# Kernel tuning notes

Hardware: AMD Instinct MI355X
Metric: run time of the kernel (lower is better)

Reference implementation:

```python
import jax, jax.numpy as jnp
import numpy as np

N_NODES = 468  # MediaPipe face-mesh landmark count


def build_edges(n):
    # static edge structure from create_face_graph: i <-> j for j in i+1..min(i+10, n)
    src, dst = [], []
    for i in range(n):
        for j in range(i + 1, min(i + 10, n)):
            src += [i, j]
            dst += [j, i]
    # PyG GCNConv adds self-loops before normalization
    src = np.asarray(src + list(range(n)), dtype=np.int32)
    dst = np.asarray(dst + list(range(n)), dtype=np.int32)
    deg = np.bincount(dst, minlength=n).astype(np.float32)
    dinv = 1.0 / np.sqrt(deg)
    norm = (dinv[src] * dinv[dst]).astype(np.float32)
    return jnp.asarray(src), jnp.asarray(dst), jnp.asarray(norm)


def gcn_conv(x, W, b, src, dst, norm):
    # x: [B, N, d_in] -> [B, N, d_out]; GCNConv: transform then normalized scatter-add
    h = x @ W                                   # [B, N, d_out]
    msg = h[:, src, :] * norm[None, :, None]    # gather along node dim: [B, E, d_out]
    agg = jnp.zeros_like(h).at[:, dst, :].add(msg)
    return agg + b


def setup_inputs() -> dict:
    key = jax.random.key(0)
    ks = jax.random.split(key, 13)
    s = 0.05
    inp = {
        'landmarks': jax.random.normal(ks[0], (128, N_NODES * 3), dtype=jnp.float32),
        'W_enc': jax.random.normal(ks[1], (3, 64), dtype=jnp.float32) * s,
        'b_enc': jnp.zeros((64,), dtype=jnp.float32),
        'W1': jax.random.normal(ks[2], (64, 128), dtype=jnp.float32) * s,
        'b1': jnp.zeros((128,), dtype=jnp.float32),
        'W2': jax.random.normal(ks[3], (128, 256), dtype=jnp.float32) * s,
        'b2': jnp.zeros((256,), dtype=jnp.float32),
        'W3': jax.random.normal(ks[4], (256, 128), dtype=jnp.float32) * s,
        'b3': jnp.zeros((128,), dtype=jnp.float32),
        'W_fus': jax.random.normal(ks[5], (128, 512), dtype=jnp.float32) * s,
        'b_fus': jnp.zeros((512,), dtype=jnp.float32),
        'W_cls': jax.random.normal(ks[6], (512, 2), dtype=jnp.float32) * s,
        'b_cls': jnp.zeros((2,), dtype=jnp.float32),
    }
    return inp


def reference(landmarks, W_enc, b_enc, W1, b1, W2, b2, W3, b3, W_fus, b_fus, W_cls, b_cls):
    B = landmarks.shape[0]
    n = landmarks.shape[1] // 3
    src, dst, norm = build_edges(n)
    x = landmarks.reshape(B, n, 3) @ W_enc + b_enc            # node encoder [B,N,64]
    x = jax.nn.relu(gcn_conv(x, W1, b1, src, dst, norm))      # [B,N,128]
    x = jax.nn.relu(gcn_conv(x, W2, b2, src, dst, norm))      # [B,N,256]
    x = jax.nn.relu(gcn_conv(x, W3, b3, src, dst, norm))      # [B,N,128]
    graph_features = jnp.mean(x, axis=1)                      # global mean pool [B,128]
    features = jax.nn.relu(graph_features @ W_fus + b_fus)    # fusion (dropout=eval) [B,512]
    output = features @ W_cls + b_cls                         # classifier [B,2]
    return output, features, graph_features
```

## Files before the change

### kernel.cpp

```cpp
#include <hip/hip_runtime.h>
#include <hip/hip_bf16.h>

typedef __bf16 bf16x8 __attribute__((ext_vector_type(8)));
typedef float  f32x4  __attribute__((ext_vector_type(4)));
typedef unsigned short ushort_t;

#define NN 468

#define W1H 0
#define W1L 8192
#define W2H 16384
#define W2L 49152
#define W3H 81920
#define W3L 114688

#define L_Y1   32096
#define L_Y2   27200
#define L_Y3   43296
#define L_LM   76352
#define L_DTAB 77768
#define L_POOL 78240

#define MFMA3(d, ah, al, wh, wl)                                        \
    d = __builtin_amdgcn_mfma_f32_16x16x32_bf16(ah, wh, d, 0, 0, 0);    \
    d = __builtin_amdgcn_mfma_f32_16x16x32_bf16(ah, wl, d, 0, 0, 0);    \
    d = __builtin_amdgcn_mfma_f32_16x16x32_bf16(al, wh, d, 0, 0, 0);

__device__ __forceinline__ void pack_split4(const float* y,
                                            ushort_t* hdst, ushort_t* ldst) {
    ushort_t h[4], l[4];
    #pragma unroll
    for (int j = 0; j < 4; ++j) {
        __hip_bfloat16 hb = __float2bfloat16(y[j]);
        float hf = __bfloat162float(hb);
        __hip_bfloat16 lb = __float2bfloat16(y[j] - hf);
        h[j] = *(ushort_t*)&hb; l[j] = *(ushort_t*)&lb;
    }
    uint2 hv = make_uint2((unsigned)h[0] | ((unsigned)h[1] << 16),
                          (unsigned)h[2] | ((unsigned)h[3] << 16));
    uint2 lv = make_uint2((unsigned)l[0] | ((unsigned)l[1] << 16),
                          (unsigned)l[2] | ((unsigned)l[3] << 16));
    *(uint2*)hdst = hv;
    *(uint2*)ldst = lv;
}

__device__ __forceinline__ int frag_off(int r, int k, int K16) {
    return (r >> 4) * K16 + (k >> 5) * 512 + ((k >> 3) & 3) * 128
         + (r & 15) * 8 + (k & 7);
}

__device__ __forceinline__ int ywoff(int r, int k4, int K16) {
    int q = (k4 >> 3) & 3;
    int u = q * 16 + (((r & 15) ^ (q << 1)) & 15);
    return (r >> 4) * K16 + (k4 >> 5) * 512 + u * 8 + (k4 & 7);
}

__global__ __launch_bounds__(512, 4) void fused(
    const float* __restrict__ Lm, const ushort_t* __restrict__ wext,
    const float* __restrict__ We, const float* __restrict__ be,
    const float* __restrict__ b1, const float* __restrict__ b2,
    const float* __restrict__ b3, float* __restrict__ partial)
{
    __shared__ __align__(16) char lds[78752];
    float*    X    = (float*)(lds);
    ushort_t* Y1h  = (ushort_t*)(lds + L_Y1);  ushort_t* Y1l = Y1h + 7168;
    ushort_t* Y2h  = (ushort_t*)(lds + L_Y2);  ushort_t* Y2l = Y2h + 12288;
    ushort_t* Y3h  = (ushort_t*)(lds + L_Y3);  ushort_t* Y3l = Y3h + 8192;
    float*    lmst = (float*)(lds + L_LM);
    float*    dtab = (float*)(lds + L_DTAB);
    float*    pool = (float*)(lds + L_POOL);

    const int tid  = threadIdx.x;
    const int lane = tid & 63;
    const int wave = tid >> 6;
    const int wm = wave & 1, wn = wave >> 1;
    const int l15 = lane & 15, lg = lane >> 4;
    const int lswz = (lane & 48) + (((lane & 15) ^ ((lane >> 4) << 1)) & 15);
    const int rt = blockIdx.x, b = blockIdx.y;
    const int r0 = rt * 64;

    if (tid < 118) {
        int ri = r0 - 27 + tid;
        float dv = 0.f;
        if (ri >= 0 && ri < NN) {
            int lo = ri - 9; if (lo < 0) lo = 0;
            int hi = ri + 9; if (hi > NN - 1) hi = NN - 1;
            dv = 1.0f / sqrtf((float)(hi - lo + 1));
        }
        dtab[tid] = dv;
    }
    if (tid < 354) {
        int g = (r0 - 27) * 3 + tid;
        lmst[tid] = (g >= 0 && g < NN * 3) ? Lm[(size_t)b * (NN * 3) + g] : 0.f;
    }
    if (tid < 128) pool[tid] = 0.f;
    __syncthreads();

    {
        const int c = tid & 63;
        const float w0 = We[c], w1 = We[64 + c], w2 = We[128 + c], bk = be[c];
        for (int l0 = tid >> 6; l0 < 118; l0 += 8) {
            float x = bk + lmst[l0*3]*w0 + lmst[l0*3+1]*w1 + lmst[l0*3+2]*w2;
            X[l0 * 68 + c] = x * dtab[l0];
        }
    }
    __syncthreads();

    {
        const int c4 = (tid & 15) << 2;
        const int base = (tid >> 4) * 4;
        if (base < 100) {
            f32x4 ws = {};
            #pragma unroll
            for (int d = 0; d < 19; ++d)
                ws += *(const f32x4*)(X + (base + d) * 68 + c4);
            #pragma unroll
            for (int rr = 0; rr < 4; ++rr) {
                int row = base + rr;
                if (rr) ws += *(const f32x4*)(X + (row + 18) * 68 + c4)
                            - *(const f32x4*)(X + (row - 1)  * 68 + c4);
                float dv = dtab[row + 9];
                float y4[4] = {ws[0]*dv, ws[1]*dv, ws[2]*dv, ws[3]*dv};
                int off = ywoff(row, c4, 1024);
                pack_split4(y4, Y1h + off, Y1l + off);
            }
        } else if (base < 112) {
            float z4[4] = {0.f, 0.f, 0.f, 0.f};
            #pragma unroll
            for (int rr = 0; rr < 4; ++rr) {
                int row = base + rr;
                if (row < 112) {
                    int off = ywoff(row, c4, 1024);
                    pack_split4(z4, Y1h + off, Y1l + off);
                }
            }
        }
    }
    __syncthreads();

    f32x4 acc1[4][2] = {};
    __builtin_amdgcn_s_setprio(1);
    #pragma unroll
    for (int kt = 0; kt < 2; ++kt) {
        bf16x8 a[4][2];
        #pragma unroll
        for (int mt = 0; mt < 4; ++mt) {
            int t = wm*4 + mt; if (t > 6) t = 6;
            int off = t * 1024 + kt * 512 + lswz * 8;
            a[mt][0] = *(const bf16x8*)(Y1h + off);
            a[mt][1] = *(const bf16x8*)(Y1l + off);
        }
        #pragma unroll
        for (int nt = 0; nt < 2; ++nt) {
            int woff = (nt*4 + wn) * 1024 + kt * 512 + lane * 8;
            bf16x8 wh = *(const bf16x8*)(wext + W1H + woff);
            bf16x8 wl = *(const bf16x8*)(wext + W1L + woff);
            #pragma unroll
            for (int mt = 0; mt < 4; ++mt) {
                MFMA3(acc1[mt][nt], a[mt][0], a[mt][1], wh, wl);
            }
        }
    }
    __builtin_amdgcn_s_setprio(0);

    #pragma unroll
    for (int kc = 0; kc < 2; ++kc) {
        #pragma unroll
        for (int mt = 0; mt < 4; ++mt) {
            int t = wm*4 + mt; if (t > 6) t = 6;
            int gcol = (kc*4 + wn)*16 + l15;
            int cl   = wn*16 + l15;
            float bv = b1[gcol];
            #pragma unroll
            for (int r = 0; r < 4; ++r) {
                int lr1 = t*16 + lg*4 + r;
                if (lr1 < 100)
                    X[lr1*68 + cl] =
                        dtab[lr1 + 9] * fmaxf(acc1[mt][kc][r] + bv, 0.f);
            }
        }
        __syncthreads();

        {
            const int c4   = (tid & 15) << 2;
            const int base = (tid >> 4) * 3;
            f32x4 ws = {};
            if (base < 82) {
                #pragma unroll
                for (int d = 0; d < 19; ++d)
                    ws += *(const f32x4*)(X + (base + d) * 68 + c4);
            }
            #pragma unroll
            for (int rr = 0; rr < 3; ++rr) {
                int row = base + rr;
                if (row < 96) {
                    float y4[4] = {0.f, 0.f, 0.f, 0.f};
                    if (row < 82) {
                        if (rr) ws += *(const f32x4*)(X + (row + 18) * 68 + c4)
                                    - *(const f32x4*)(X + (row - 1)  * 68 + c4);
                        float dv = dtab[row + 18];
                        y4[0] = ws[0]*dv; y4[1] = ws[1]*dv;
                        y4[2] = ws[2]*dv; y4[3] = ws[3]*dv;
                    }
                    int off = ywoff(row, kc*64 + c4, 2048);
                    pack_split4(y4, Y2h + off, Y2l + off);
                }
            }
        }
        __syncthreads();
    }

    f32x4 acc2[3][4] = {};
    __builtin_amdgcn_s_setprio(1);
    #pragma unroll
    for (int kt = 0; kt < 4; ++kt) {
        bf16x8 a[3][2];
        #pragma unroll
        for (int mt = 0; mt < 3; ++mt) {
            int off = (wm*3 + mt) * 2048 + kt * 512 + lswz * 8;
            a[mt][0] = *(const bf16x8*)(Y2h + off);
            a[mt][1] = *(const bf16x8*)(Y2l + off);
        }
        #pragma unroll
        for (int nt = 0; nt < 4; ++nt) {
            int woff = (nt*4 + wn) * 2048 + kt * 512 + lane * 8;
            bf16x8 wh = *(const bf16x8*)(wext + W2H + woff);
            bf16x8 wl = *(const bf16x8*)(wext + W2L + woff);
            #pragma unroll
            for (int mt = 0; mt < 3; ++mt) {
                MFMA3(acc2[mt][nt], a[mt][0], a[mt][1], wh, wl);
            }
        }
    }
    __builtin_amdgcn_s_setprio(0);
    __syncthreads();

    f32x4 acc3[2][2] = {};
    #pragma unroll
    for (int nc = 0; nc < 2; ++nc) {
        if (nc == 1) {
            __builtin_amdgcn_s_setprio(1);
            #pragma unroll
            for (int kt = 0; kt < 4; ++kt) {
                bf16x8 a0[2], a1[2];
                #pragma unroll
                for (int mt = 0; mt < 2; ++mt) {
                    int aoff = (wm*2 + mt) * 2048 + kt * 512 + lswz * 8;
                    a0[mt] = *(const bf16x8*)(Y3h + aoff);
                    a1[mt] = *(const bf16x8*)(Y3l + aoff);
                }
                #pragma unroll
                for (int nt = 0; nt < 2; ++nt) {
                    int woff = (nt*4 + wn) * 4096 + (0*4 + kt) * 512 + lane * 8;
                    bf16x8 wh = *(const bf16x8*)(wext + W3H + woff);
                    bf16x8 wl = *(const bf16x8*)(wext + W3L + woff);
                    #pragma unroll
                    for (int mt = 0; mt < 2; ++mt) {
                        MFMA3(acc3[mt][nt], a0[mt], a1[mt], wh, wl);
                    }
                }
            }
            __builtin_amdgcn_s_setprio(0);
        }
        #pragma unroll
        for (int mt = 0; mt < 3; ++mt)
        #pragma unroll
        for (int q = 0; q < 2; ++q) {
            int gcol = ((nc*2 + q)*4 + wn)*16 + l15;
            int cl   = (q*4 + wn)*16 + l15;
            float bv = b2[gcol];
            #pragma unroll
            for (int r = 0; r < 4; ++r) {
                int lr2 = (wm*3 + mt)*16 + lg*4 + r;
                if (lr2 < 82)
                    X[lr2*132 + cl] =
                        dtab[lr2 + 18] * fmaxf(acc2[mt][nc*2 + q][r] + bv, 0.f);
            }
        }
        __syncthreads();

        {
            const int c4   = (tid & 31) << 2;
            const int base = (tid >> 5) * 4;
            f32x4 ws = {};
            #pragma unroll
            for (int d = 0; d < 19; ++d)
                ws += *(const f32x4*)(X + (base + d) * 132 + c4);
            #pragma unroll
            for (int rr = 0; rr < 4; ++rr) {
                int row = base + rr;
                if (rr) ws += *(const f32x4*)(X + (row + 18) * 132 + c4)
                            - *(const f32x4*)(X + (row - 1)  * 132 + c4);
                float dv = dtab[row + 27];
                float y4[4] = {ws[0]*dv, ws[1]*dv, ws[2]*dv, ws[3]*dv};
                int off = ywoff(row, c4, 2048);
                pack_split4(y4, Y3h + off, Y3l + off);
            }
        }
        __syncthreads();
    }

    __builtin_amdgcn_s_setprio(1);
    #pragma unroll
    for (int kt = 0; kt < 4; ++kt) {
        bf16x8 a0[2], a1[2];
        #pragma unroll
        for (int mt = 0; mt < 2; ++mt) {
            int aoff = (wm*2 + mt) * 2048 + kt * 512 + lswz * 8;
            a0[mt] = *(const bf16x8*)(Y3h + aoff);
            a1[mt] = *(const bf16x8*)(Y3l + aoff);
        }
        #pragma unroll
        for (int nt = 0; nt < 2; ++nt) {
            int woff = (nt*4 + wn) * 4096 + (1*4 + kt) * 512 + lane * 8;
            bf16x8 wh = *(const bf16x8*)(wext + W3H + woff);
            bf16x8 wl = *(const bf16x8*)(wext + W3L + woff);
            #pragma unroll
            for (int mt = 0; mt < 2; ++mt) {
                MFMA3(acc3[mt][nt], a0[mt], a1[mt], wh, wl);
            }
        }
    }
    __builtin_amdgcn_s_setprio(0);

    #pragma unroll
    for (int nt = 0; nt < 2; ++nt) {
        int g_t = nt*4 + wn;
        float bv = b3[g_t*16 + l15];
        float cs = 0.f;
        #pragma unroll
        for (int mt = 0; mt < 2; ++mt)
        #pragma unroll
        for (int r = 0; r < 4; ++r) {
            int gr = r0 + (wm*2 + mt)*16 + lg*4 + r;
            if (gr < NN) cs += fmaxf(acc3[mt][nt][r] + bv, 0.f);
        }
        cs += __shfl_xor(cs, 16);
        cs += __shfl_xor(cs, 32);
        if (lane < 16) atomicAdd(&pool[g_t*16 + lane], cs);
    }
    __syncthreads();
    if (tid < 128) partial[((size_t)b * 8 + rt) * 128 + tid] = pool[tid];
}

__global__ __launch_bounds__(256) void wconv(
    const float* __restrict__ W1, const float* __restrict__ W2,
    const float* __restrict__ W3, ushort_t* __restrict__ wext)
{
    int i = blockIdx.x * 256 + threadIdx.x;
    float w; int off_h, off_l, idx;
    if (i < 8192) {
        int k = i >> 7, n = i & 127;
        w = W1[i]; idx = frag_off(n, k, 1024);  off_h = W1H; off_l = W1L;
    } else if (i < 40960) {
        int j = i - 8192;
        int k = j >> 8, n = j & 255;
        w = W2[j]; idx = frag_off(n, k, 2048);  off_h = W2H; off_l = W2L;
    } else if (i < 73728) {
        int j = i - 40960;
        int k = j >> 7, n = j & 127;
        w = W3[j]; idx = frag_off(n, k, 4096);  off_h = W3H; off_l = W3L;
    } else return;
    __hip_bfloat16 hb = __float2bfloat16(w);
    float hf = __bfloat162float(hb);
    __hip_bfloat16 lb = __float2bfloat16(w - hf);
    wext[off_h + idx] = *(ushort_t*)&hb;
    wext[off_l + idx] = *(ushort_t*)&lb;
}

__global__ __launch_bounds__(512) void head_kernel(
    const float* __restrict__ partial, const float* __restrict__ Wf,
    const float* __restrict__ bf, const float* __restrict__ Wc,
    const float* __restrict__ bc, float* __restrict__ dout)
{
    __shared__ float gfs[128];
    __shared__ float feats[512];
    int b = blockIdx.x, t = threadIdx.x;
    if (t < 128) {
        const float* p = partial + (size_t)b * (8 * 128);
        float s = 0.f;
        #pragma unroll
        for (int tt = 0; tt < 8; ++tt) s += p[tt * 128 + t];
        s *= (1.0f / 468.0f);
        gfs[t] = s;
        dout[65792 + b * 128 + t] = s;
    }
    __syncthreads();
    float a = bf[t];
    for (int k = 0; k < 128; ++k) a += gfs[k] * Wf[k * 512 + t];
    a = fmaxf(a, 0.f);
    dout[256 + b * 512 + t] = a;
    feats[t] = a;
    __syncthreads();
    if (t < 64) {
        float s0 = 0.f, s1 = 0.f;
        for (int c = t; c < 512; c += 64) {
            float f = feats[c];
            s0 += f * Wc[c * 2 + 0];
            s1 += f * Wc[c * 2 + 1];
        }
        #pragma unroll
        for (int off = 32; off; off >>= 1) {
            s0 += __shfl_down(s0, off);
            s1 += __shfl_down(s1, off);
        }
        if (t == 0) {
            dout[b * 2 + 0] = s0 + bc[0];
            dout[b * 2 + 1] = s1 + bc[1];
        }
    }
}

extern "C" void kernel_launch(void* const* d_in, const int* in_sizes, int n_in,
                              void* d_out, int out_size, void* d_ws, size_t ws_size,
                              hipStream_t stream)
{
    const float* landmarks = (const float*)d_in[0];
    const float* W_enc     = (const float*)d_in[1];
    const float* b_enc     = (const float*)d_in[2];
    const float* W1        = (const float*)d_in[3];
    const float* b1        = (const float*)d_in[4];
    const float* W2        = (const float*)d_in[5];
    const float* b2        = (const float*)d_in[6];
    const float* W3        = (const float*)d_in[7];
    const float* b3        = (const float*)d_in[8];
    const float* W_fus     = (const float*)d_in[9];
    const float* b_fus     = (const float*)d_in[10];
    const float* W_cls     = (const float*)d_in[11];
    const float* b_cls     = (const float*)d_in[12];
    float* out = (float*)d_out;

    char* ws = (char*)d_ws;
    ushort_t* wext = (ushort_t*)(ws + 0);
    float* partial = (float*)(ws + 294912);

    wconv<<<288, 256, 0, stream>>>(W1, W2, W3, wext);
    fused<<<dim3(8, 128), 512, 0, stream>>>(
        landmarks, wext, W_enc, b_enc, b1, b2, b3, partial);
    head_kernel<<<128, 512, 0, stream>>>(partial, W_fus, b_fus, W_cls, b_cls, out);
}
```

Baseline: 66.79 us.

## Process two batch samples per block with interleaved software-pipelined phases

Each block now handles two batch elements, with double LDS buffers, and interleaves the phases of the two samples so one sample's GEMM runs alongside the other's band/epilogue work between barriers. The aim is to hide the LDS/ALU phases behind MFMA work and cut the number of barrier-serialized stalls per sample. The cost is doubled LDS (about 157KB, so one block per CU), more live accumulators, and half the grid size, which may reduce occupancy and latency hiding.

```diff
diff --git a/kernel.cpp b/kernel.cpp
--- a/kernel.cpp
+++ b/kernel.cpp
@@ -14,12 +14,14 @@
 #define W3H 81920
 #define W3L 114688
 
-#define L_Y1   32096
-#define L_Y2   27200
-#define L_Y3   43296
-#define L_LM   76352
-#define L_DTAB 77768
-#define L_POOL 78240
+#define UO_Y1 32096
+#define UO_Y2 27200
+#define UO_Y3 43296
+#define UO_LM 76352
+#define U_STRIDE 77768
+#define L_DTAB  (2*U_STRIDE)
+#define L_POOLA (L_DTAB + 472)
+#define L_POOLB (L_POOLA + 512)
 
 #define MFMA3(d, ah, al, wh, wl)                                        \
     d = __builtin_amdgcn_mfma_f32_16x16x32_bf16(ah, wh, d, 0, 0, 0);    \
@@ -55,31 +57,11 @@
     return (r >> 4) * K16 + (k4 >> 5) * 512 + u * 8 + (k4 & 7);
 }
 
-__global__ __launch_bounds__(512, 4) void fused(
-    const float* __restrict__ Lm, const ushort_t* __restrict__ wext,
-    const float* __restrict__ We, const float* __restrict__ be,
-    const float* __restrict__ b1, const float* __restrict__ b2,
-    const float* __restrict__ b3, float* __restrict__ partial)
-{
-    __shared__ __align__(16) char lds[78752];
-    float*    X    = (float*)(lds);
-    ushort_t* Y1h  = (ushort_t*)(lds + L_Y1);  ushort_t* Y1l = Y1h + 7168;
-    ushort_t* Y2h  = (ushort_t*)(lds + L_Y2);  ushort_t* Y2l = Y2h + 12288;
-    ushort_t* Y3h  = (ushort_t*)(lds + L_Y3);  ushort_t* Y3l = Y3h + 8192;
-    float*    lmst = (float*)(lds + L_LM);
-    float*    dtab = (float*)(lds + L_DTAB);
-    float*    pool = (float*)(lds + L_POOL);
-
-    const int tid  = threadIdx.x;
-    const int lane = tid & 63;
-    const int wave = tid >> 6;
-    const int wm = wave & 1, wn = wave >> 1;
-    const int l15 = lane & 15, lg = lane >> 4;
-    const int lswz = (lane & 48) + (((lane & 15) ^ ((lane >> 4) << 1)) & 15);
-    const int rt = blockIdx.x, b = blockIdx.y;
-    const int r0 = rt * 64;
-
-    if (tid < 118) {
+__device__ __forceinline__ void ph_stage(const float* Lm, float* lmst,
+                                         float* pool, float* dtab, bool do_dtab,
+                                         int b, int r0) {
+    int tid = threadIdx.x;
+    if (do_dtab && tid < 118) {
         int ri = r0 - 27 + tid;
         float dv = 0.f;
         if (ri >= 0 && ri < NN) {
@@ -94,51 +76,59 @@
         lmst[tid] = (g >= 0 && g < NN * 3) ? Lm[(size_t)b * (NN * 3) + g] : 0.f;
     }
     if (tid < 128) pool[tid] = 0.f;
-    __syncthreads();
-
-    {
-        const int c = tid & 63;
-        const float w0 = We[c], w1 = We[64 + c], w2 = We[128 + c], bk = be[c];
-        for (int l0 = tid >> 6; l0 < 118; l0 += 8) {
-            float x = bk + lmst[l0*3]*w0 + lmst[l0*3+1]*w1 + lmst[l0*3+2]*w2;
-            X[l0 * 68 + c] = x * dtab[l0];
-        }
-    }
-    __syncthreads();
-
-    {
-        const int c4 = (tid & 15) << 2;
-        const int base = (tid >> 4) * 4;
-        if (base < 100) {
-            f32x4 ws = {};
-            #pragma unroll
-            for (int d = 0; d < 19; ++d)
-                ws += *(const f32x4*)(X + (base + d) * 68 + c4);
-            #pragma unroll
-            for (int rr = 0; rr < 4; ++rr) {
-                int row = base + rr;
-                if (rr) ws += *(const f32x4*)(X + (row + 18) * 68 + c4)
-                            - *(const f32x4*)(X + (row - 1)  * 68 + c4);
-                float dv = dtab[row + 9];
-                float y4[4] = {ws[0]*dv, ws[1]*dv, ws[2]*dv, ws[3]*dv};
+}
+
+__device__ __forceinline__ void ph_enc(float* X, const float* lmst,
+                                       const float* dtab, const float* We,
+                                       const float* be) {
+    int tid = threadIdx.x;
+    const int c = tid & 63;
+    const float w0 = We[c], w1 = We[64 + c], w2 = We[128 + c], bk = be[c];
+    for (int l0 = tid >> 6; l0 < 118; l0 += 8) {
+        float x = bk + lmst[l0*3]*w0 + lmst[l0*3+1]*w1 + lmst[l0*3+2]*w2;
+        X[l0 * 68 + c] = x * dtab[l0];
+    }
+}
+
+__device__ __forceinline__ void ph_band1(const float* X, ushort_t* Y1h,
+                                         ushort_t* Y1l, const float* dtab) {
+    int tid = threadIdx.x;
+    const int c4 = (tid & 15) << 2;
+    const int base = (tid >> 4) * 4;
+    if (base < 100) {
+        f32x4 ws = {};
+        #pragma unroll
+        for (int d = 0; d < 19; ++d)
+            ws += *(const f32x4*)(X + (base + d) * 68 + c4);
+        #pragma unroll
+        for (int rr = 0; rr < 4; ++rr) {
+            int row = base + rr;
+            if (rr) ws += *(const f32x4*)(X + (row + 18) * 68 + c4)
+                        - *(const f32x4*)(X + (row - 1)  * 68 + c4);
+            float dv = dtab[row + 9];
+            float y4[4] = {ws[0]*dv, ws[1]*dv, ws[2]*dv, ws[3]*dv};
+            int off = ywoff(row, c4, 1024);
+            pack_split4(y4, Y1h + off, Y1l + off);
+        }
+    } else if (base < 112) {
+        float z4[4] = {0.f, 0.f, 0.f, 0.f};
+        #pragma unroll
+        for (int rr = 0; rr < 4; ++rr) {
+            int row = base + rr;
+            if (row < 112) {
                 int off = ywoff(row, c4, 1024);
-                pack_split4(y4, Y1h + off, Y1l + off);
+                pack_split4(z4, Y1h + off, Y1l + off);
             }
-        } else if (base < 112) {
-            float z4[4] = {0.f, 0.f, 0.f, 0.f};
-            #pragma unroll
-            for (int rr = 0; rr < 4; ++rr) {
-                int row = base + rr;
-                if (row < 112) {
-                    int off = ywoff(row, c4, 1024);
-                    pack_split4(z4, Y1h + off, Y1l + off);
-                }
-            }
-        }
-    }
-    __syncthreads();
-
-    f32x4 acc1[4][2] = {};
+        }
+    }
+}
+
+__device__ __forceinline__ void ph_gemm1(const ushort_t* Y1h, const ushort_t* Y1l,
+                                         const ushort_t* wext, f32x4 (&acc1)[4][2]) {
+    int tid = threadIdx.x;
+    const int lane = tid & 63, wave = tid >> 6;
+    const int wm = wave & 1, wn = wave >> 1;
+    const int lswz = (lane & 48) + (((lane & 15) ^ ((lane >> 4) << 1)) & 15);
     __builtin_amdgcn_s_setprio(1);
     #pragma unroll
     for (int kt = 0; kt < 2; ++kt) {
@@ -162,55 +152,64 @@
         }
     }
     __builtin_amdgcn_s_setprio(0);
-
-    #pragma unroll
-    for (int kc = 0; kc < 2; ++kc) {
-        #pragma unroll
-        for (int mt = 0; mt < 4; ++mt) {
-            int t = wm*4 + mt; if (t > 6) t = 6;
-            int gcol = (kc*4 + wn)*16 + l15;
-            int cl   = wn*16 + l15;
-            float bv = b1[gcol];
-            #pragma unroll
-            for (int r = 0; r < 4; ++r) {
-                int lr1 = t*16 + lg*4 + r;
-                if (lr1 < 100)
-                    X[lr1*68 + cl] =
-                        dtab[lr1 + 9] * fmaxf(acc1[mt][kc][r] + bv, 0.f);
+}
+
+__device__ __forceinline__ void ph_epi1(float* X, const f32x4 (&acc1)[4][2],
+                                        const float* dtab, const float* b1, int kc) {
+    int tid = threadIdx.x;
+    const int lane = tid & 63, wave = tid >> 6;
+    const int wm = wave & 1, wn = wave >> 1;
+    const int l15 = lane & 15, lg = lane >> 4;
+    #pragma unroll
+    for (int mt = 0; mt < 4; ++mt) {
+        int t = wm*4 + mt; if (t > 6) t = 6;
+        int gcol = (kc*4 + wn)*16 + l15;
+        int cl   = wn*16 + l15;
+        float bv = b1[gcol];
+        #pragma unroll
+        for (int r = 0; r < 4; ++r) {
+            int lr1 = t*16 + lg*4 + r;
+            if (lr1 < 100)
+                X[lr1*68 + cl] = dtab[lr1 + 9] * fmaxf(acc1[mt][kc][r] + bv, 0.f);
+        }
+    }
+}
+
+__device__ __forceinline__ void ph_band2(const float* X, ushort_t* Y2h,
+                                         ushort_t* Y2l, const float* dtab, int kc) {
+    int tid = threadIdx.x;
+    const int c4   = (tid & 15) << 2;
+    const int base = (tid >> 4) * 3;
+    f32x4 ws = {};
+    if (base < 82) {
+        #pragma unroll
+        for (int d = 0; d < 19; ++d)
+            ws += *(const f32x4*)(X + (base + d) * 68 + c4);
+    }
+    #pragma unroll
+    for (int rr = 0; rr < 3; ++rr) {
+        int row = base + rr;
+        if (row < 96) {
+            float y4[4] = {0.f, 0.f, 0.f, 0.f};
+            if (row < 82) {
+                if (rr) ws += *(const f32x4*)(X + (row + 18) * 68 + c4)
+                            - *(const f32x4*)(X + (row - 1)  * 68 + c4);
+                float dv = dtab[row + 18];
+                y4[0] = ws[0]*dv; y4[1] = ws[1]*dv;
+                y4[2] = ws[2]*dv; y4[3] = ws[3]*dv;
             }
-        }
-        __syncthreads();
-
-        {
-            const int c4   = (tid & 15) << 2;
-            const int base = (tid >> 4) * 3;
-            f32x4 ws = {};
-            if (base < 82) {
-                #pragma unroll
-                for (int d = 0; d < 19; ++d)
-                    ws += *(const f32x4*)(X + (base + d) * 68 + c4);
-            }
-            #pragma unroll
-            for (int rr = 0; rr < 3; ++rr) {
-                int row = base + rr;
-                if (row < 96) {
-                    float y4[4] = {0.f, 0.f, 0.f, 0.f};
-                    if (row < 82) {
-                        if (rr) ws += *(const f32x4*)(X + (row + 18) * 68 + c4)
-                                    - *(const f32x4*)(X + (row - 1)  * 68 + c4);
-                        float dv = dtab[row + 18];
-                        y4[0] = ws[0]*dv; y4[1] = ws[1]*dv;
-                        y4[2] = ws[2]*dv; y4[3] = ws[3]*dv;
-                    }
-                    int off = ywoff(row, kc*64 + c4, 2048);
-                    pack_split4(y4, Y2h + off, Y2l + off);
-                }
-            }
-        }
-        __syncthreads();
-    }
-
-    f32x4 acc2[3][4] = {};
+            int off = ywoff(row, kc*64 + c4, 2048);
+            pack_split4(y4, Y2h + off, Y2l + off);
+        }
+    }
+}
+
+__device__ __forceinline__ void ph_gemm2(const ushort_t* Y2h, const ushort_t* Y2l,
+                                         const ushort_t* wext, f32x4 (&acc2)[3][4]) {
+    int tid = threadIdx.x;
+    const int lane = tid & 63, wave = tid >> 6;
+    const int wm = wave & 1, wn = wave >> 1;
+    const int lswz = (lane & 48) + (((lane & 15) ^ ((lane >> 4) << 1)) & 15);
     __builtin_amdgcn_s_setprio(1);
     #pragma unroll
     for (int kt = 0; kt < 4; ++kt) {
@@ -233,73 +232,58 @@
         }
     }
     __builtin_amdgcn_s_setprio(0);
-    __syncthreads();
-
-    f32x4 acc3[2][2] = {};
-    #pragma unroll
-    for (int nc = 0; nc < 2; ++nc) {
-        if (nc == 1) {
-            __builtin_amdgcn_s_setprio(1);
-            #pragma unroll
-            for (int kt = 0; kt < 4; ++kt) {
-                bf16x8 a0[2], a1[2];
-                #pragma unroll
-                for (int mt = 0; mt < 2; ++mt) {
-                    int aoff = (wm*2 + mt) * 2048 + kt * 512 + lswz * 8;
-                    a0[mt] = *(const bf16x8*)(Y3h + aoff);
-                    a1[mt] = *(const bf16x8*)(Y3l + aoff);
-                }
-                #pragma unroll
-                for (int nt = 0; nt < 2; ++nt) {
-                    int woff = (nt*4 + wn) * 4096 + (0*4 + kt) * 512 + lane * 8;
-                    bf16x8 wh = *(const bf16x8*)(wext + W3H + woff);
-                    bf16x8 wl = *(const bf16x8*)(wext + W3L + woff);
-                    #pragma unroll
-                    for (int mt = 0; mt < 2; ++mt) {
-                        MFMA3(acc3[mt][nt], a0[mt], a1[mt], wh, wl);
-                    }
-                }
-            }
-            __builtin_amdgcn_s_setprio(0);
-        }
-        #pragma unroll
-        for (int mt = 0; mt < 3; ++mt)
-        #pragma unroll
-        for (int q = 0; q < 2; ++q) {
-            int gcol = ((nc*2 + q)*4 + wn)*16 + l15;
-            int cl   = (q*4 + wn)*16 + l15;
-            float bv = b2[gcol];
-            #pragma unroll
-            for (int r = 0; r < 4; ++r) {
-                int lr2 = (wm*3 + mt)*16 + lg*4 + r;
-                if (lr2 < 82)
-                    X[lr2*132 + cl] =
-                        dtab[lr2 + 18] * fmaxf(acc2[mt][nc*2 + q][r] + bv, 0.f);
-            }
-        }
-        __syncthreads();
-
-        {
-            const int c4   = (tid & 31) << 2;
-            const int base = (tid >> 5) * 4;
-            f32x4 ws = {};
-            #pragma unroll
-            for (int d = 0; d < 19; ++d)
-                ws += *(const f32x4*)(X + (base + d) * 132 + c4);
-            #pragma unroll
-            for (int rr = 0; rr < 4; ++rr) {
-                int row = base + rr;
-                if (rr) ws += *(const f32x4*)(X + (row + 18) * 132 + c4)
-                            - *(const f32x4*)(X + (row - 1)  * 132 + c4);
-                float dv = dtab[row + 27];
-                float y4[4] = {ws[0]*dv, ws[1]*dv, ws[2]*dv, ws[3]*dv};
-                int off = ywoff(row, c4, 2048);
-                pack_split4(y4, Y3h + off, Y3l + off);
-            }
-        }
-        __syncthreads();
-    }
-
+}
+
+__device__ __forceinline__ void ph_epi2(float* X, const f32x4 (&acc2)[3][4],
+                                        const float* dtab, const float* b2, int nc) {
+    int tid = threadIdx.x;
+    const int lane = tid & 63, wave = tid >> 6;
+    const int wm = wave & 1, wn = wave >> 1;
+    const int l15 = lane & 15, lg = lane >> 4;
+    #pragma unroll
+    for (int mt = 0; mt < 3; ++mt)
+    #pragma unroll
+    for (int q = 0; q < 2; ++q) {
+        int gcol = ((nc*2 + q)*4 + wn)*16 + l15;
+        int cl   = (q*4 + wn)*16 + l15;
+        float bv = b2[gcol];
+        #pragma unroll
+        for (int r = 0; r < 4; ++r) {
+            int lr2 = (wm*3 + mt)*16 + lg*4 + r;
+            if (lr2 < 82)
+                X[lr2*132 + cl] = dtab[lr2 + 18] * fmaxf(acc2[mt][nc*2 + q][r] + bv, 0.f);
+        }
+    }
+}
+
+__device__ __forceinline__ void ph_band3(const float* X, ushort_t* Y3h,
+                                         ushort_t* Y3l, const float* dtab) {
+    int tid = threadIdx.x;
+    const int c4   = (tid & 31) << 2;
+    const int base = (tid >> 5) * 4;
+    f32x4 ws = {};
+    #pragma unroll
+    for (int d = 0; d < 19; ++d)
+        ws += *(const f32x4*)(X + (base + d) * 132 + c4);
+    #pragma unroll
+    for (int rr = 0; rr < 4; ++rr) {
+        int row = base + rr;
+        if (rr) ws += *(const f32x4*)(X + (row + 18) * 132 + c4)
+                    - *(const f32x4*)(X + (row - 1)  * 132 + c4);
+        float dv = dtab[row + 27];
+        float y4[4] = {ws[0]*dv, ws[1]*dv, ws[2]*dv, ws[3]*dv};
+        int off = ywoff(row, c4, 2048);
+        pack_split4(y4, Y3h + off, Y3l + off);
+    }
+}
+
+__device__ __forceinline__ void ph_gemm3(const ushort_t* Y3h, const ushort_t* Y3l,
+                                         const ushort_t* wext, f32x4 (&acc3)[2][2],
+                                         int nc) {
+    int tid = threadIdx.x;
+    const int lane = tid & 63, wave = tid >> 6;
+    const int wm = wave & 1, wn = wave >> 1;
+    const int lswz = (lane & 48) + (((lane & 15) ^ ((lane >> 4) << 1)) & 15);
     __builtin_amdgcn_s_setprio(1);
     #pragma unroll
     for (int kt = 0; kt < 4; ++kt) {
@@ -312,7 +296,7 @@
         }
         #pragma unroll
         for (int nt = 0; nt < 2; ++nt) {
-            int woff = (nt*4 + wn) * 4096 + (1*4 + kt) * 512 + lane * 8;
+            int woff = (nt*4 + wn) * 4096 + (nc*4 + kt) * 512 + lane * 8;
             bf16x8 wh = *(const bf16x8*)(wext + W3H + woff);
             bf16x8 wl = *(const bf16x8*)(wext + W3L + woff);
             #pragma unroll
@@ -322,7 +306,15 @@
         }
     }
     __builtin_amdgcn_s_setprio(0);
-
+}
+
+__device__ __forceinline__ void ph_pool(const f32x4 (&acc3)[2][2], float* pool,
+                                        const float* b3, float* partial,
+                                        int b, int rt, int r0) {
+    int tid = threadIdx.x;
+    const int lane = tid & 63, wave = tid >> 6;
+    const int wm = wave & 1, wn = wave >> 1;
+    const int l15 = lane & 15, lg = lane >> 4;
     #pragma unroll
     for (int nt = 0; nt < 2; ++nt) {
         int g_t = nt*4 + wn;
@@ -341,6 +333,72 @@
     }
     __syncthreads();
     if (tid < 128) partial[((size_t)b * 8 + rt) * 128 + tid] = pool[tid];
+}
+
+__global__ __launch_bounds__(512, 2) void fused2(
+    const float* __restrict__ Lm, const ushort_t* __restrict__ wext,
+    const float* __restrict__ We, const float* __restrict__ be,
+    const float* __restrict__ b1, const float* __restrict__ b2,
+    const float* __restrict__ b3, float* __restrict__ partial)
+{
+    __shared__ __align__(16) char lds[157056];
+    char* uA = lds;
+    char* uB = lds + U_STRIDE;
+    float*    XA   = (float*)(uA);
+    ushort_t* Y1hA = (ushort_t*)(uA + UO_Y1);  ushort_t* Y1lA = Y1hA + 7168;
+    ushort_t* Y2hA = (ushort_t*)(uA + UO_Y2);  ushort_t* Y2lA = Y2hA + 12288;
+    ushort_t* Y3hA = (ushort_t*)(uA + UO_Y3);  ushort_t* Y3lA = Y3hA + 8192;
+    float*    lmA  = (float*)(uA + UO_LM);
+    float*    XB   = (float*)(uB);
+    ushort_t* Y1hB = (ushort_t*)(uB + UO_Y1);  ushort_t* Y1lB = Y1hB + 7168;
+    ushort_t* Y2hB = (ushort_t*)(uB + UO_Y2);  ushort_t* Y2lB = Y2hB + 12288;
+    ushort_t* Y3hB = (ushort_t*)(uB + UO_Y3);  ushort_t* Y3lB = Y3hB + 8192;
+    float*    lmB  = (float*)(uB + UO_LM);
+    float*    dtab = (float*)(lds + L_DTAB);
+    float*    poolA = (float*)(lds + L_POOLA);
+    float*    poolB = (float*)(lds + L_POOLB);
+
+    const int rt = blockIdx.x;
+    const int bA = blockIdx.y * 2, bB = bA + 1;
+    const int r0 = rt * 64;
+
+    f32x4 acc1A[4][2] = {}; f32x4 acc2A[3][4] = {}; f32x4 acc3A[2][2] = {};
+    f32x4 acc1B[4][2] = {}; f32x4 acc2B[3][4] = {}; f32x4 acc3B[2][2] = {};
+
+    #define BAR __syncthreads()
+    ph_stage(Lm, lmA, poolA, dtab, true, bA, r0);                    BAR;
+    ph_enc(XA, lmA, dtab, We, be);                                   BAR;
+    ph_band1(XA, Y1hA, Y1lA, dtab);                                  BAR;
+    ph_gemm1(Y1hA, Y1lA, wext, acc1A);                               BAR;
+    ph_epi1(XA, acc1A, dtab, b1, 0);                                 BAR;
+    ph_band2(XA, Y2hA, Y2lA, dtab, 0);
+    ph_stage(Lm, lmB, poolB, dtab, false, bB, r0);                   BAR;
+    ph_epi1(XA, acc1A, dtab, b1, 1);
+    ph_enc(XB, lmB, dtab, We, be);                                   BAR;
+    ph_band2(XA, Y2hA, Y2lA, dtab, 1);
+    ph_band1(XB, Y1hB, Y1lB, dtab);                                  BAR;
+    ph_gemm2(Y2hA, Y2lA, wext, acc2A);
+    ph_gemm1(Y1hB, Y1lB, wext, acc1B);                               BAR;
+    ph_epi2(XA, acc2A, dtab, b2, 0);
+    ph_epi1(XB, acc1B, dtab, b1, 0);                                 BAR;
+    ph_band3(XA, Y3hA, Y3lA, dtab);
+    ph_band2(XB, Y2hB, Y2lB, dtab, 0);                               BAR;
+    ph_gemm3(Y3hA, Y3lA, wext, acc3A, 0);
+    ph_epi1(XB, acc1B, dtab, b1, 1);                                 BAR;
+    ph_epi2(XA, acc2A, dtab, b2, 1);
+    ph_band2(XB, Y2hB, Y2lB, dtab, 1);                               BAR;
+    ph_band3(XA, Y3hA, Y3lA, dtab);
+    ph_gemm2(Y2hB, Y2lB, wext, acc2B);                               BAR;
+    ph_gemm3(Y3hA, Y3lA, wext, acc3A, 1);
+    ph_epi2(XB, acc2B, dtab, b2, 0);                                 BAR;
+    ph_pool(acc3A, poolA, b3, partial, bA, rt, r0);
+    ph_band3(XB, Y3hB, Y3lB, dtab);                                  BAR;
+    ph_gemm3(Y3hB, Y3lB, wext, acc3B, 0);                            BAR;
+    ph_epi2(XB, acc2B, dtab, b2, 1);                                 BAR;
+    ph_band3(XB, Y3hB, Y3lB, dtab);                                  BAR;
+    ph_gemm3(Y3hB, Y3lB, wext, acc3B, 1);                            BAR;
+    ph_pool(acc3B, poolB, b3, partial, bB, rt, r0);
+    #undef BAR
 }
 
 __global__ __launch_bounds__(256) void wconv(
@@ -435,7 +493,7 @@
     float* partial = (float*)(ws + 294912);
 
     wconv<<<288, 256, 0, stream>>>(W1, W2, W3, wext);
-    fused<<<dim3(8, 128), 512, 0, stream>>>(
+    fused2<<<dim3(8, 64), 512, 0, stream>>>(
         landmarks, wext, W_enc, b_enc, b1, b2, b3, partial);
     head_kernel<<<128, 512, 0, stream>>>(partial, W_fus, b_fus, W_cls, b_cls, out);
 }
```

Result: slower. 148.1 us (+121.8%).

## Double fused kernel block size to 1024 threads, splitting N-tiles across waves

Applied to the files above, without the earlier changes.

Raises the fused GCN kernel from 512 to 1024 threads per block, so 16 waves each own half as many output column tiles in every MFMA stage and half as many rows in the sliding-window aggregation passes. The aim is more parallelism and latency hiding per block, with fewer accumulator registers per thread. The cost is lower possible blocks per CU given the large LDS footprint and the register limit that launch_bounds(1024,4) imposes, and more waves contending at each barrier. Some stages, such as the layer-1 epilogue, now leave half the waves idle.

```diff
diff --git a/kernel.cpp b/kernel.cpp
--- a/kernel.cpp
+++ b/kernel.cpp
@@ -55,7 +55,7 @@
     return (r >> 4) * K16 + (k4 >> 5) * 512 + u * 8 + (k4 & 7);
 }
 
-__global__ __launch_bounds__(512, 4) void fused(
+__global__ __launch_bounds__(1024, 4) void fused(
     const float* __restrict__ Lm, const ushort_t* __restrict__ wext,
     const float* __restrict__ We, const float* __restrict__ be,
     const float* __restrict__ b1, const float* __restrict__ b2,
@@ -99,7 +99,7 @@
     {
         const int c = tid & 63;
         const float w0 = We[c], w1 = We[64 + c], w2 = We[128 + c], bk = be[c];
-        for (int l0 = tid >> 6; l0 < 118; l0 += 8) {
+        for (int l0 = tid >> 6; l0 < 118; l0 += 16) {
             float x = bk + lmst[l0*3]*w0 + lmst[l0*3+1]*w1 + lmst[l0*3+2]*w2;
             X[l0 * 68 + c] = x * dtab[l0];
         }
@@ -108,14 +108,14 @@
 
     {
         const int c4 = (tid & 15) << 2;
-        const int base = (tid >> 4) * 4;
+        const int base = (tid >> 4) * 2;
         if (base < 100) {
             f32x4 ws = {};
             #pragma unroll
             for (int d = 0; d < 19; ++d)
                 ws += *(const f32x4*)(X + (base + d) * 68 + c4);
             #pragma unroll
-            for (int rr = 0; rr < 4; ++rr) {
+            for (int rr = 0; rr < 2; ++rr) {
                 int row = base + rr;
                 if (rr) ws += *(const f32x4*)(X + (row + 18) * 68 + c4)
                             - *(const f32x4*)(X + (row - 1)  * 68 + c4);
@@ -127,7 +127,7 @@
         } else if (base < 112) {
             float z4[4] = {0.f, 0.f, 0.f, 0.f};
             #pragma unroll
-            for (int rr = 0; rr < 4; ++rr) {
+            for (int rr = 0; rr < 2; ++rr) {
                 int row = base + rr;
                 if (row < 112) {
                     int off = ywoff(row, c4, 1024);
@@ -138,7 +138,7 @@
     }
     __syncthreads();
 
-    f32x4 acc1[4][2] = {};
+    f32x4 acc1[4] = {};
     __builtin_amdgcn_s_setprio(1);
     #pragma unroll
     for (int kt = 0; kt < 2; ++kt) {
@@ -150,67 +150,68 @@
             a[mt][0] = *(const bf16x8*)(Y1h + off);
             a[mt][1] = *(const bf16x8*)(Y1l + off);
         }
-        #pragma unroll
-        for (int nt = 0; nt < 2; ++nt) {
-            int woff = (nt*4 + wn) * 1024 + kt * 512 + lane * 8;
-            bf16x8 wh = *(const bf16x8*)(wext + W1H + woff);
-            bf16x8 wl = *(const bf16x8*)(wext + W1L + woff);
+        int woff = wn * 1024 + kt * 512 + lane * 8;
+        bf16x8 wh = *(const bf16x8*)(wext + W1H + woff);
+        bf16x8 wl = *(const bf16x8*)(wext + W1L + woff);
+        #pragma unroll
+        for (int mt = 0; mt < 4; ++mt) {
+            MFMA3(acc1[mt], a[mt][0], a[mt][1], wh, wl);
+        }
+    }
+    __builtin_amdgcn_s_setprio(0);
+
+    #pragma unroll
+    for (int kc = 0; kc < 2; ++kc) {
+        if ((wn >> 2) == kc) {
+            int gcol = wn*16 + l15;
+            int cl   = (wn & 3)*16 + l15;
+            float bv = b1[gcol];
             #pragma unroll
             for (int mt = 0; mt < 4; ++mt) {
-                MFMA3(acc1[mt][nt], a[mt][0], a[mt][1], wh, wl);
-            }
-        }
-    }
-    __builtin_amdgcn_s_setprio(0);
-
-    #pragma unroll
-    for (int kc = 0; kc < 2; ++kc) {
-        #pragma unroll
-        for (int mt = 0; mt < 4; ++mt) {
-            int t = wm*4 + mt; if (t > 6) t = 6;
-            int gcol = (kc*4 + wn)*16 + l15;
-            int cl   = wn*16 + l15;
-            float bv = b1[gcol];
-            #pragma unroll
-            for (int r = 0; r < 4; ++r) {
-                int lr1 = t*16 + lg*4 + r;
-                if (lr1 < 100)
-                    X[lr1*68 + cl] =
-                        dtab[lr1 + 9] * fmaxf(acc1[mt][kc][r] + bv, 0.f);
+                int t = wm*4 + mt; if (t > 6) t = 6;
+                #pragma unroll
+                for (int r = 0; r < 4; ++r) {
+                    int lr1 = t*16 + lg*4 + r;
+                    if (lr1 < 100)
+                        X[lr1*68 + cl] =
+                            dtab[lr1 + 9] * fmaxf(acc1[mt][r] + bv, 0.f);
+                }
             }
         }
         __syncthreads();
 
         {
             const int c4   = (tid & 15) << 2;
-            const int base = (tid >> 4) * 3;
-            f32x4 ws = {};
-            if (base < 82) {
+            const int base = (tid >> 4) * 2;
+            if (base < 96) {
+                f32x4 ws = {};
+                if (base < 82) {
+                    #pragma unroll
+                    for (int d = 0; d < 19; ++d)
+                        ws += *(const f32x4*)(X + (base + d) * 68 + c4);
+                }
                 #pragma unroll
-                for (int d = 0; d < 19; ++d)
-                    ws += *(const f32x4*)(X + (base + d) * 68 + c4);
-            }
-            #pragma unroll
-            for (int rr = 0; rr < 3; ++rr) {
-                int row = base + rr;
-                if (row < 96) {
-                    float y4[4] = {0.f, 0.f, 0.f, 0.f};
-                    if (row < 82) {
-                        if (rr) ws += *(const f32x4*)(X + (row + 18) * 68 + c4)
-                                    - *(const f32x4*)(X + (row - 1)  * 68 + c4);
-                        float dv = dtab[row + 18];
-                        y4[0] = ws[0]*dv; y4[1] = ws[1]*dv;
-                        y4[2] = ws[2]*dv; y4[3] = ws[3]*dv;
+                for (int rr = 0; rr < 2; ++rr) {
+                    int row = base + rr;
+                    if (row < 96) {
+                        float y4[4] = {0.f, 0.f, 0.f, 0.f};
+                        if (row < 82) {
+                            if (rr) ws += *(const f32x4*)(X + (row + 18) * 68 + c4)
+                                        - *(const f32x4*)(X + (row - 1)  * 68 + c4);
+                            float dv = dtab[row + 18];
+                            y4[0] = ws[0]*dv; y4[1] = ws[1]*dv;
+                            y4[2] = ws[2]*dv; y4[3] = ws[3]*dv;
+                        }
+                        int off = ywoff(row, kc*64 + c4, 2048);
+                        pack_split4(y4, Y2h + off, Y2l + off);
                     }
-                    int off = ywoff(row, kc*64 + c4, 2048);
-                    pack_split4(y4, Y2h + off, Y2l + off);
                 }
             }
         }
         __syncthreads();
     }
 
-    f32x4 acc2[3][4] = {};
+    f32x4 acc2[3][2] = {};
     __builtin_amdgcn_s_setprio(1);
     #pragma unroll
     for (int kt = 0; kt < 4; ++kt) {
@@ -222,8 +223,8 @@
             a[mt][1] = *(const bf16x8*)(Y2l + off);
         }
         #pragma unroll
-        for (int nt = 0; nt < 4; ++nt) {
-            int woff = (nt*4 + wn) * 2048 + kt * 512 + lane * 8;
+        for (int nt = 0; nt < 2; ++nt) {
+            int woff = (nt*8 + wn) * 2048 + kt * 512 + lane * 8;
             bf16x8 wh = *(const bf16x8*)(wext + W2H + woff);
             bf16x8 wl = *(const bf16x8*)(wext + W2L + woff);
             #pragma unroll
@@ -235,7 +236,7 @@
     __builtin_amdgcn_s_setprio(0);
     __syncthreads();
 
-    f32x4 acc3[2][2] = {};
+    f32x4 acc3[2] = {};
     #pragma unroll
     for (int nc = 0; nc < 2; ++nc) {
         if (nc == 1) {
@@ -249,45 +250,41 @@
                     a0[mt] = *(const bf16x8*)(Y3h + aoff);
                     a1[mt] = *(const bf16x8*)(Y3l + aoff);
                 }
+                int woff = wn * 4096 + (0*4 + kt) * 512 + lane * 8;
+                bf16x8 wh = *(const bf16x8*)(wext + W3H + woff);
+                bf16x8 wl = *(const bf16x8*)(wext + W3L + woff);
                 #pragma unroll
-                for (int nt = 0; nt < 2; ++nt) {
-                    int woff = (nt*4 + wn) * 4096 + (0*4 + kt) * 512 + lane * 8;
-                    bf16x8 wh = *(const bf16x8*)(wext + W3H + woff);
-                    bf16x8 wl = *(const bf16x8*)(wext + W3L + woff);
-                    #pragma unroll
-                    for (int mt = 0; mt < 2; ++mt) {
-                        MFMA3(acc3[mt][nt], a0[mt], a1[mt], wh, wl);
-                    }
+                for (int mt = 0; mt < 2; ++mt) {
+                    MFMA3(acc3[mt], a0[mt], a1[mt], wh, wl);
                 }
             }
             __builtin_amdgcn_s_setprio(0);
         }
-        #pragma unroll
-        for (int mt = 0; mt < 3; ++mt)
-        #pragma unroll
-        for (int q = 0; q < 2; ++q) {
-            int gcol = ((nc*2 + q)*4 + wn)*16 + l15;
-            int cl   = (q*4 + wn)*16 + l15;
+        {
+            int gcol = (nc*8 + wn)*16 + l15;
+            int cl   = wn*16 + l15;
             float bv = b2[gcol];
+            #pragma unroll
+            for (int mt = 0; mt < 3; ++mt)
             #pragma unroll
             for (int r = 0; r < 4; ++r) {
                 int lr2 = (wm*3 + mt)*16 + lg*4 + r;
                 if (lr2 < 82)
                     X[lr2*132 + cl] =
-                        dtab[lr2 + 18] * fmaxf(acc2[mt][nc*2 + q][r] + bv, 0.f);
+                        dtab[lr2 + 18] * fmaxf(acc2[mt][nc][r] + bv, 0.f);
             }
         }
         __syncthreads();
 
         {
             const int c4   = (tid & 31) << 2;
-            const int base = (tid >> 5) * 4;
+            const int base = (tid >> 5) * 2;
             f32x4 ws = {};
             #pragma unroll
             for (int d = 0; d < 19; ++d)
                 ws += *(const f32x4*)(X + (base + d) * 132 + c4);
             #pragma unroll
-            for (int rr = 0; rr < 4; ++rr) {
+            for (int rr = 0; rr < 2; ++rr) {
                 int row = base + rr;
                 if (rr) ws += *(const f32x4*)(X + (row + 18) * 132 + c4)
                             - *(const f32x4*)(X + (row - 1)  * 132 + c4);
@@ -310,34 +307,29 @@
             a0[mt] = *(const bf16x8*)(Y3h + aoff);
             a1[mt] = *(const bf16x8*)(Y3l + aoff);
         }
-        #pragma unroll
-        for (int nt = 0; nt < 2; ++nt) {
-            int woff = (nt*4 + wn) * 4096 + (1*4 + kt) * 512 + lane * 8;
-            bf16x8 wh = *(const bf16x8*)(wext + W3H + woff);
-            bf16x8 wl = *(const bf16x8*)(wext + W3L + woff);
-            #pragma unroll
-            for (int mt = 0; mt < 2; ++mt) {
-                MFMA3(acc3[mt][nt], a0[mt], a1[mt], wh, wl);
-            }
+        int woff = wn * 4096 + (1*4 + kt) * 512 + lane * 8;
+        bf16x8 wh = *(const bf16x8*)(wext + W3H + woff);
+        bf16x8 wl = *(const bf16x8*)(wext + W3L + woff);
+        #pragma unroll
+        for (int mt = 0; mt < 2; ++mt) {
+            MFMA3(acc3[mt], a0[mt], a1[mt], wh, wl);
         }
     }
     __builtin_amdgcn_s_setprio(0);
 
-    #pragma unroll
-    for (int nt = 0; nt < 2; ++nt) {
-        int g_t = nt*4 + wn;
-        float bv = b3[g_t*16 + l15];
+    {
+        float bv = b3[wn*16 + l15];
         float cs = 0.f;
         #pragma unroll
         for (int mt = 0; mt < 2; ++mt)
         #pragma unroll
         for (int r = 0; r < 4; ++r) {
             int gr = r0 + (wm*2 + mt)*16 + lg*4 + r;
-            if (gr < NN) cs += fmaxf(acc3[mt][nt][r] + bv, 0.f);
+            if (gr < NN) cs += fmaxf(acc3[mt][r] + bv, 0.f);
         }
         cs += __shfl_xor(cs, 16);
         cs += __shfl_xor(cs, 32);
-        if (lane < 16) atomicAdd(&pool[g_t*16 + lane], cs);
+        if (lane < 16) atomicAdd(&pool[wn*16 + lane], cs);
     }
     __syncthreads();
     if (tid < 128) partial[((size_t)b * 8 + rt) * 128 + tid] = pool[tid];
@@ -435,7 +427,7 @@
     float* partial = (float*)(ws + 294912);
 
     wconv<<<288, 256, 0, stream>>>(W1, W2, W3, wext);
-    fused<<<dim3(8, 128), 512, 0, stream>>>(
+    fused<<<dim3(8, 128), 1024, 0, stream>>>(
         landmarks, wext, W_enc, b_enc, b1, b2, b3, partial);
     head_kernel<<<128, 512, 0, stream>>>(partial, W_fus, b_fus, W_cls, b_cls, out);
 }
```

Result: slower. 83.73 us (+25.4%).
